# Performance work log

Measured on AMD Instinct MI355X. Metric: run time of the kernel, lower is better.

Reference implementation:

```python
import jax, jax.numpy as jnp
import numpy as np

B, W, H, I, L = 64, 4096, 128, 128, 2


def setup_inputs() -> dict:
    key = jax.random.key(0)
    ks = jax.random.split(key, 16)
    f = lambda k, s: jax.random.normal(k, s, dtype=jnp.float32) * 0.05
    return dict(
        input=f(ks[0], (B, 1, I)),
        h0=f(ks[1], (L, B, H)),
        c0=f(ks[2], (L, B, H)),
        encoder_output=f(ks[3], (B, W, H)),
        att_W=f(ks[4], (1, 2 * H)), att_b=f(ks[5], (1,)),
        inp_W=f(ks[6], (I, H + I)), inp_b=f(ks[7], (I,)),
        W_ih0=f(ks[8], (4 * H, I)), W_hh0=f(ks[9], (4 * H, H)),
        b_ih0=f(ks[10], (4 * H,)), b_hh0=f(ks[11], (4 * H,)),
        W_ih1=f(ks[12], (4 * H, H)), W_hh1=f(ks[13], (4 * H, H)),
        b_ih1=f(ks[14], (4 * H,)), b_hh1=f(ks[15], (4 * H,)),
    )


def _lstm_cell(x, h, c, W_ih, W_hh, b_ih, b_hh):
    # PyTorch gate order: i, f, g, o
    gates = x @ W_ih.T + h @ W_hh.T + b_ih + b_hh
    i, f, g, o = jnp.split(gates, 4, axis=-1)
    c_new = jax.nn.sigmoid(f) * c + jax.nn.sigmoid(i) * jnp.tanh(g)
    h_new = jax.nn.sigmoid(o) * jnp.tanh(c_new)
    return h_new, c_new


def reference(input, h0, c0, encoder_output, att_W, att_b, inp_W, inp_b,
              W_ih0, W_hh0, b_ih0, b_hh0, W_ih1, W_hh1, b_ih1, b_hh1):
    att_state = h0[-1] * c0[-1]                       # (B, H)
    # att_line over concat(enc_word, att_state): split the (1, 2H) weight.
    wa_enc, wa_st = att_W[0, :H], att_W[0, H:]
    scores = encoder_output @ wa_enc + (att_state @ wa_st + att_b[0])[:, None]  # (B, W)
    # Faithful to original: a leading zeros column is prepended, then
    # softmax is taken over [:, 0:-1] -> keeps the zero column, drops the
    # LAST word's score.
    zero_col = jnp.zeros((scores.shape[0], 1), scores.dtype)
    full = jnp.concatenate([zero_col, scores], axis=1)  # (B, W+1)
    weight = jax.nn.softmax(full[:, :-1], axis=1)        # (B, W)
    x = jnp.einsum('bw,bwh->bh', weight, encoder_output)  # (B, H)
    xin = jnp.concatenate([x, input[:, 0, :]], axis=1) @ inp_W.T + inp_b  # (B, I)
    # 2-layer LSTM, single time step (eval mode -> inter-layer dropout off)
    h1, c1 = _lstm_cell(xin, h0[0], c0[0], W_ih0, W_hh0, b_ih0, b_hh0)
    h2, c2 = _lstm_cell(h1, h0[1], c0[1], W_ih1, W_hh1, b_ih1, b_hh1)
    output = h2[:, None, :]                              # (B, 1, H)
    return output, jnp.stack([h1, h2]), jnp.stack([c1, c2])
```

## Files before the change

kernel.cpp:

```cpp
#include <hip/hip_runtime.h>

#define BB 64
#define WW 4096
#define HH 128
#define NCHUNK 32
#define CROWS 128
#define PSTRIDE 132

__device__ inline float sigmoidf(float x) { return 1.0f / (1.0f + expf(-x)); }

__global__ void fused_attention(const float* __restrict__ enc,
                                const float* __restrict__ h0,
                                const float* __restrict__ c0,
                                const float* __restrict__ attW,
                                const float* __restrict__ attb,
                                float* __restrict__ partials) {
    __shared__ float s_wa[128];
    __shared__ float s_red[128];
    __shared__ float s_sc[CROWS];
    __shared__ float s_p[CROWS];
    __shared__ float racc[16 * 128];
    __shared__ float s_bias, s_m, s_extra;

    const int t = threadIdx.x;
    const int b = blockIdx.x >> 5;
    const int chunk = blockIdx.x & 31;
    const int w0 = chunk * CROWS;

    const int seg = t & 15;
    const int rg  = t >> 4;

    float4 ra[8], rc[8];
#pragma unroll
    for (int pass = 0; pass < 8; pass++) {
        const int r = pass * 16 + rg;
        const float4* p = (const float4*)(enc + ((size_t)b * WW + w0 + r) * HH + seg * 8);
        ra[pass] = p[0];
        rc[pass] = p[1];
    }

    if (t < 128) {
        s_wa[t] = attW[t];
        float hv = h0[BB * HH + b * HH + t];
        float cv = c0[BB * HH + b * HH + t];
        s_red[t] = hv * cv * attW[HH + t];
    }
    __syncthreads();
    for (int s = 64; s > 0; s >>= 1) {
        if (t < s) s_red[t] += s_red[t + s];
        __syncthreads();
    }
    if (t == 0) s_bias = s_red[0] + attb[0];
    __syncthreads();
    const float bias = s_bias;

    float wseg[8];
#pragma unroll
    for (int j = 0; j < 8; j++) wseg[j] = s_wa[seg * 8 + j];

#pragma unroll
    for (int pass = 0; pass < 8; pass++) {
        const int r = pass * 16 + rg;
        float d = ra[pass].x * wseg[0] + ra[pass].y * wseg[1]
                + ra[pass].z * wseg[2] + ra[pass].w * wseg[3]
                + rc[pass].x * wseg[4] + rc[pass].y * wseg[5]
                + rc[pass].z * wseg[6] + rc[pass].w * wseg[7];
        d += __shfl_xor(d, 8, 16);
        d += __shfl_xor(d, 4, 16);
        d += __shfl_xor(d, 2, 16);
        d += __shfl_xor(d, 1, 16);
        if (seg == 0) s_sc[r] = d + bias;
    }

    if (chunk > 0 && t < 16) {
        const float4* p = (const float4*)(enc + ((size_t)b * WW + w0 - 1) * HH + t * 8);
        float4 a = p[0], c = p[1];
        float d = a.x * wseg[0] + a.y * wseg[1] + a.z * wseg[2] + a.w * wseg[3]
                + c.x * wseg[4] + c.y * wseg[5] + c.z * wseg[6] + c.w * wseg[7];
        d += __shfl_xor(d, 8, 16);
        d += __shfl_xor(d, 4, 16);
        d += __shfl_xor(d, 2, 16);
        d += __shfl_xor(d, 1, 16);
        if (t == 0) s_extra = d + bias;
    }
    __syncthreads();

    if (t < 128) {
        float v;
        if (t == 0) v = (chunk > 0) ? s_extra : -1e30f;
        else        v = s_sc[t - 1];
        s_p[t] = v;
    }
    __syncthreads();

    if (t < 64) s_red[t] = fmaxf(s_p[t], s_p[t + 64]);
    __syncthreads();
    for (int s = 32; s > 0; s >>= 1) {
        if (t < s) s_red[t] = fmaxf(s_red[t], s_red[t + s]);
        __syncthreads();
    }
    if (t == 0) s_m = s_red[0];
    __syncthreads();
    const float m = s_m;

    if (t < 128) s_p[t] = expf(s_p[t] - m);
    __syncthreads();
    if (t < 64) s_red[t] = s_p[t] + s_p[t + 64];
    __syncthreads();
    for (int s = 32; s > 0; s >>= 1) {
        if (t < s) s_red[t] += s_red[t + s];
        __syncthreads();
    }

    float acc8[8];
#pragma unroll
    for (int j = 0; j < 8; j++) acc8[j] = 0.f;
#pragma unroll
    for (int pass = 0; pass < 8; pass++) {
        const int r = pass * 16 + rg;
        const float pw = s_p[r];
        acc8[0] += pw * ra[pass].x; acc8[1] += pw * ra[pass].y;
        acc8[2] += pw * ra[pass].z; acc8[3] += pw * ra[pass].w;
        acc8[4] += pw * rc[pass].x; acc8[5] += pw * rc[pass].y;
        acc8[6] += pw * rc[pass].z; acc8[7] += pw * rc[pass].w;
    }
#pragma unroll
    for (int j = 0; j < 8; j++) racc[rg * 128 + seg * 8 + j] = acc8[j];
    __syncthreads();

    float* out = partials + (size_t)(b * NCHUNK + chunk) * PSTRIDE;
    if (t < 128) {
        float s = 0.f;
#pragma unroll
        for (int w2 = 0; w2 < 16; w2++) s += racc[w2 * 128 + t];
        out[t] = s;
    }
    if (t == 128) out[128] = m;
    if (t == 129) out[129] = s_red[0];
}

__global__ void tail_kernel(const float* __restrict__ partials,
                            const float* __restrict__ enc,
                            const float* __restrict__ input,
                            const float* __restrict__ inpW,
                            const float* __restrict__ inpb,
                            const float* __restrict__ Wih0,
                            const float* __restrict__ Whh0,
                            const float* __restrict__ bih0,
                            const float* __restrict__ bhh0,
                            const float* __restrict__ Wih1,
                            const float* __restrict__ Whh1,
                            const float* __restrict__ bih1,
                            const float* __restrict__ bhh1,
                            const float* __restrict__ h0,
                            const float* __restrict__ c0,
                            float* __restrict__ out) {
    __shared__ float lm[NCHUNK], llv[NCHUNK], ls[NCHUNK];
    __shared__ float sM, sL;
    __shared__ float xc[256];
    __shared__ float sxv[128];
    __shared__ float shv[128];
    __shared__ float sh1[128];
    __shared__ float shv2[128];
    __shared__ float gates[512];

    const int b = blockIdx.x;
    const int t = threadIdx.x;

    if (t < NCHUNK) {
        const float* pp = partials + (size_t)(b * NCHUNK + t) * PSTRIDE;
        lm[t] = pp[128];
        llv[t] = pp[129];
    }
    __syncthreads();
    if (t == 0) {
        float M = 0.0f;
        for (int c = 0; c < NCHUNK; c++) M = fmaxf(M, lm[c]);
        float L = expf(-M);
        for (int c = 0; c < NCHUNK; c++) {
            float s = expf(lm[c] - M);
            ls[c] = s;
            L += s * llv[c];
        }
        sM = M; sL = L;
    }
    __syncthreads();

    if (t < 128) {
        float xv = expf(-sM) * enc[(size_t)b * WW * HH + t];
        for (int c = 0; c < NCHUNK; c++)
            xv += ls[c] * partials[(size_t)(b * NCHUNK + c) * PSTRIDE + t];
        xc[t] = xv / sL;
        xc[128 + t] = input[b * HH + t];
    }
    __syncthreads();

    if (t < 128) {
        float a = inpb[t];
        const float4* wr = (const float4*)(inpW + (size_t)t * 256);
#pragma unroll
        for (int k = 0; k < 64; k++) {
            float4 w4 = wr[k];
            a += xc[4 * k] * w4.x + xc[4 * k + 1] * w4.y
               + xc[4 * k + 2] * w4.z + xc[4 * k + 3] * w4.w;
        }
        sxv[t] = a;
        shv[t] = h0[b * HH + t];
        shv2[t] = h0[BB * HH + b * HH + t];
    }
    __syncthreads();

    {
        float g = bih0[t] + bhh0[t];
        const float4* wi = (const float4*)(Wih0 + (size_t)t * 128);
        const float4* wh = (const float4*)(Whh0 + (size_t)t * 128);
#pragma unroll
        for (int k = 0; k < 32; k++) {
            float4 a = wi[k], c = wh[k];
            g += sxv[4 * k] * a.x + sxv[4 * k + 1] * a.y + sxv[4 * k + 2] * a.z + sxv[4 * k + 3] * a.w
               + shv[4 * k] * c.x + shv[4 * k + 1] * c.y + shv[4 * k + 2] * c.z + shv[4 * k + 3] * c.w;
        }
        gates[t] = g;
    }
    __syncthreads();
    if (t < 128) {
        float ig = sigmoidf(gates[t]);
        float fg = sigmoidf(gates[128 + t]);
        float gg = tanhf(gates[256 + t]);
        float og = sigmoidf(gates[384 + t]);
        float cn = fg * c0[b * HH + t] + ig * gg;
        float hn = og * tanhf(cn);
        out[8192 + b * HH + t] = hn;
        out[24576 + b * HH + t] = cn;
        sh1[t] = hn;
    }
    __syncthreads();

    {
        float g = bih1[t] + bhh1[t];
        const float4* wi = (const float4*)(Wih1 + (size_t)t * 128);
        const float4* wh = (const float4*)(Whh1 + (size_t)t * 128);
#pragma unroll
        for (int k = 0; k < 32; k++) {
            float4 a = wi[k], c = wh[k];
            g += sh1[4 * k] * a.x + sh1[4 * k + 1] * a.y + sh1[4 * k + 2] * a.z + sh1[4 * k + 3] * a.w
               + shv2[4 * k] * c.x + shv2[4 * k + 1] * c.y + shv2[4 * k + 2] * c.z + shv2[4 * k + 3] * c.w;
        }
        gates[t] = g;
    }
    __syncthreads();
    if (t < 128) {
        float ig = sigmoidf(gates[t]);
        float fg = sigmoidf(gates[128 + t]);
        float gg = tanhf(gates[256 + t]);
        float og = sigmoidf(gates[384 + t]);
        float cn = fg * c0[BB * HH + b * HH + t] + ig * gg;
        float hn = og * tanhf(cn);
        out[b * HH + t] = hn;
        out[16384 + b * HH + t] = hn;
        out[32768 + b * HH + t] = cn;
    }
}

extern "C" void kernel_launch(void* const* d_in, const int* in_sizes, int n_in,
                              void* d_out, int out_size, void* d_ws, size_t ws_size,
                              hipStream_t stream) {
    const float* input = (const float*)d_in[0];
    const float* h0    = (const float*)d_in[1];
    const float* c0    = (const float*)d_in[2];
    const float* enc   = (const float*)d_in[3];
    const float* attW  = (const float*)d_in[4];
    const float* attb  = (const float*)d_in[5];
    const float* inpW  = (const float*)d_in[6];
    const float* inpb  = (const float*)d_in[7];
    const float* Wih0  = (const float*)d_in[8];
    const float* Whh0  = (const float*)d_in[9];
    const float* bih0  = (const float*)d_in[10];
    const float* bhh0  = (const float*)d_in[11];
    const float* Wih1  = (const float*)d_in[12];
    const float* Whh1  = (const float*)d_in[13];
    const float* bih1  = (const float*)d_in[14];
    const float* bhh1  = (const float*)d_in[15];

    float* partials = (float*)d_ws;

    fused_attention<<<BB * NCHUNK, 256, 0, stream>>>(enc, h0, c0, attW, attb, partials);
    tail_kernel<<<BB, 512, 0, stream>>>(partials, enc, input, inpW, inpb,
                                        Wih0, Whh0, bih0, bhh0,
                                        Wih1, Whh1, bih1, bhh1,
                                        h0, c0, (float*)d_out);
}
```

Measured before the change: 273.4 us.

## Replace shared-memory tree reductions with wavefront shuffles and split tail work across threads

The attention kernel swaps its barrier-heavy shared-memory tree reductions (bias, max, sum) for 64-lane wavefront shuffle reductions, and shrinks the 16-row partial accumulation buffer by first reducing within each wave via shuffles. The halo-row load is issued early, next to the main loads. In the tail kernel, the per-chunk max and sum become a 32-lane shuffle reduction, and the chunk combine and input projection are split across all 512 threads with a small reduction, replacing 128-thread serial loops. The aim is to cut __syncthreads count and LDS traffic, and to make the tail less serial. The cost is extra shuffle instructions and more reduction steps.

```diff
diff --git a/kernel.cpp b/kernel.cpp
--- a/kernel.cpp
+++ b/kernel.cpp
@@ -16,11 +16,11 @@
                                 const float* __restrict__ attb,
                                 float* __restrict__ partials) {
     __shared__ float s_wa[128];
-    __shared__ float s_red[128];
+    __shared__ float s_red[8];
     __shared__ float s_sc[CROWS];
     __shared__ float s_p[CROWS];
-    __shared__ float racc[16 * 128];
-    __shared__ float s_bias, s_m, s_extra;
+    __shared__ float4 racc4[128];
+    __shared__ float s_extra;
 
     const int t = threadIdx.x;
     const int b = blockIdx.x >> 5;
@@ -29,6 +29,7 @@
 
     const int seg = t & 15;
     const int rg  = t >> 4;
+    const int wv  = t >> 6;
 
     float4 ra[8], rc[8];
 #pragma unroll
@@ -38,21 +39,28 @@
         ra[pass] = p[0];
         rc[pass] = p[1];
     }
+    float4 xa = {0.f,0.f,0.f,0.f}, xb = {0.f,0.f,0.f,0.f};
+    if (chunk > 0 && t < 16) {
+        const float4* p = (const float4*)(enc + ((size_t)b * WW + w0 - 1) * HH + t * 8);
+        xa = p[0];
+        xb = p[1];
+    }
 
     if (t < 128) {
         s_wa[t] = attW[t];
         float hv = h0[BB * HH + b * HH + t];
         float cv = c0[BB * HH + b * HH + t];
-        s_red[t] = hv * cv * attW[HH + t];
-    }
-    __syncthreads();
-    for (int s = 64; s > 0; s >>= 1) {
-        if (t < s) s_red[t] += s_red[t + s];
-        __syncthreads();
-    }
-    if (t == 0) s_bias = s_red[0] + attb[0];
-    __syncthreads();
-    const float bias = s_bias;
+        float r = hv * cv * attW[HH + t];
+        r += __shfl_xor(r, 32);
+        r += __shfl_xor(r, 16);
+        r += __shfl_xor(r, 8);
+        r += __shfl_xor(r, 4);
+        r += __shfl_xor(r, 2);
+        r += __shfl_xor(r, 1);
+        if ((t & 63) == 0) s_red[wv] = r;
+    }
+    __syncthreads();
+    const float bias = s_red[0] + s_red[1] + attb[0];
 
     float wseg[8];
 #pragma unroll
@@ -73,10 +81,8 @@
     }
 
     if (chunk > 0 && t < 16) {
-        const float4* p = (const float4*)(enc + ((size_t)b * WW + w0 - 1) * HH + t * 8);
-        float4 a = p[0], c = p[1];
-        float d = a.x * wseg[0] + a.y * wseg[1] + a.z * wseg[2] + a.w * wseg[3]
-                + c.x * wseg[4] + c.y * wseg[5] + c.z * wseg[6] + c.w * wseg[7];
+        float d = xa.x * wseg[0] + xa.y * wseg[1] + xa.z * wseg[2] + xa.w * wseg[3]
+                + xb.x * wseg[4] + xb.y * wseg[5] + xb.z * wseg[6] + xb.w * wseg[7];
         d += __shfl_xor(d, 8, 16);
         d += __shfl_xor(d, 4, 16);
         d += __shfl_xor(d, 2, 16);
@@ -85,32 +91,35 @@
     }
     __syncthreads();
 
-    if (t < 128) {
-        float v;
+    float v = -1e30f;
+    if (t < 128) {
         if (t == 0) v = (chunk > 0) ? s_extra : -1e30f;
         else        v = s_sc[t - 1];
-        s_p[t] = v;
-    }
-    __syncthreads();
-
-    if (t < 64) s_red[t] = fmaxf(s_p[t], s_p[t + 64]);
-    __syncthreads();
-    for (int s = 32; s > 0; s >>= 1) {
-        if (t < s) s_red[t] = fmaxf(s_red[t], s_red[t + s]);
-        __syncthreads();
-    }
-    if (t == 0) s_m = s_red[0];
-    __syncthreads();
-    const float m = s_m;
-
-    if (t < 128) s_p[t] = expf(s_p[t] - m);
-    __syncthreads();
-    if (t < 64) s_red[t] = s_p[t] + s_p[t + 64];
-    __syncthreads();
-    for (int s = 32; s > 0; s >>= 1) {
-        if (t < s) s_red[t] += s_red[t + s];
-        __syncthreads();
-    }
+        float mv = v;
+        mv = fmaxf(mv, __shfl_xor(mv, 32));
+        mv = fmaxf(mv, __shfl_xor(mv, 16));
+        mv = fmaxf(mv, __shfl_xor(mv, 8));
+        mv = fmaxf(mv, __shfl_xor(mv, 4));
+        mv = fmaxf(mv, __shfl_xor(mv, 2));
+        mv = fmaxf(mv, __shfl_xor(mv, 1));
+        if ((t & 63) == 0) s_red[2 + wv] = mv;
+    }
+    __syncthreads();
+    const float m = fmaxf(s_red[2], s_red[3]);
+
+    if (t < 128) {
+        float p = expf(v - m);
+        s_p[t] = p;
+        float sv = p;
+        sv += __shfl_xor(sv, 32);
+        sv += __shfl_xor(sv, 16);
+        sv += __shfl_xor(sv, 8);
+        sv += __shfl_xor(sv, 4);
+        sv += __shfl_xor(sv, 2);
+        sv += __shfl_xor(sv, 1);
+        if ((t & 63) == 0) s_red[4 + wv] = sv;
+    }
+    __syncthreads();
 
     float acc8[8];
 #pragma unroll
@@ -125,18 +134,27 @@
         acc8[6] += pw * rc[pass].z; acc8[7] += pw * rc[pass].w;
     }
 #pragma unroll
-    for (int j = 0; j < 8; j++) racc[rg * 128 + seg * 8 + j] = acc8[j];
+    for (int j = 0; j < 8; j++) {
+        acc8[j] += __shfl_xor(acc8[j], 16);
+        acc8[j] += __shfl_xor(acc8[j], 32);
+    }
+    if ((t & 63) < 16) {
+        float4 lo = {acc8[0], acc8[1], acc8[2], acc8[3]};
+        float4 hi = {acc8[4], acc8[5], acc8[6], acc8[7]};
+        racc4[wv * 32 + seg * 2 + 0] = lo;
+        racc4[wv * 32 + seg * 2 + 1] = hi;
+    }
     __syncthreads();
 
     float* out = partials + (size_t)(b * NCHUNK + chunk) * PSTRIDE;
     if (t < 128) {
-        float s = 0.f;
-#pragma unroll
-        for (int w2 = 0; w2 < 16; w2++) s += racc[w2 * 128 + t];
-        out[t] = s;
-    }
-    if (t == 128) out[128] = m;
-    if (t == 129) out[129] = s_red[0];
+        const float* rf = (const float*)racc4;
+        out[t] = rf[t] + rf[128 + t] + rf[256 + t] + rf[384 + t];
+    } else if (t == 128) {
+        out[128] = m;
+    } else if (t == 129) {
+        out[129] = s_red[4] + s_red[5];
+    }
 }
 
 __global__ void tail_kernel(const float* __restrict__ partials,
@@ -155,58 +173,86 @@
                             const float* __restrict__ h0,
                             const float* __restrict__ c0,
                             float* __restrict__ out) {
-    __shared__ float lm[NCHUNK], llv[NCHUNK], ls[NCHUNK];
+    __shared__ float lm[NCHUNK], ls[NCHUNK];
     __shared__ float sM, sL;
     __shared__ float xc[256];
     __shared__ float sxv[128];
     __shared__ float shv[128];
     __shared__ float sh1[128];
     __shared__ float shv2[128];
-    __shared__ float gates[512];
+    __shared__ float red4[512];
 
     const int b = blockIdx.x;
     const int t = threadIdx.x;
-
+    const int hc = t & 127;
+    const int q  = t >> 7;
+
+    float myllv = 0.f;
     if (t < NCHUNK) {
         const float* pp = partials + (size_t)(b * NCHUNK + t) * PSTRIDE;
         lm[t] = pp[128];
-        llv[t] = pp[129];
-    }
-    __syncthreads();
-    if (t == 0) {
-        float M = 0.0f;
-        for (int c = 0; c < NCHUNK; c++) M = fmaxf(M, lm[c]);
-        float L = expf(-M);
-        for (int c = 0; c < NCHUNK; c++) {
-            float s = expf(lm[c] - M);
-            ls[c] = s;
-            L += s * llv[c];
+        myllv = pp[129];
+    } else if (t >= 128 && t < 256) {
+        shv[hc] = h0[b * HH + hc];
+    } else if (t >= 256 && t < 384) {
+        shv2[hc] = h0[BB * HH + b * HH + hc];
+    } else if (t >= 384) {
+        xc[128 + hc] = input[b * HH + hc];
+    }
+    __syncthreads();
+
+    if (t < NCHUNK) {
+        float mv = lm[t];
+        mv = fmaxf(mv, __shfl_xor(mv, 16, 32));
+        mv = fmaxf(mv, __shfl_xor(mv, 8, 32));
+        mv = fmaxf(mv, __shfl_xor(mv, 4, 32));
+        mv = fmaxf(mv, __shfl_xor(mv, 2, 32));
+        mv = fmaxf(mv, __shfl_xor(mv, 1, 32));
+        mv = fmaxf(mv, 0.0f);
+        float s = expf(lm[t] - mv);
+        ls[t] = s;
+        float L = s * myllv;
+        L += __shfl_xor(L, 16, 32);
+        L += __shfl_xor(L, 8, 32);
+        L += __shfl_xor(L, 4, 32);
+        L += __shfl_xor(L, 2, 32);
+        L += __shfl_xor(L, 1, 32);
+        if (t == 0) { sM = mv; sL = L + expf(-mv); }
+    }
+    __syncthreads();
+
+    {
+        float xv = 0.f;
+#pragma unroll
+        for (int c = 0; c < 8; c++) {
+            const int cc = q * 8 + c;
+            xv += ls[cc] * partials[(size_t)(b * NCHUNK + cc) * PSTRIDE + hc];
         }
-        sM = M; sL = L;
-    }
-    __syncthreads();
-
-    if (t < 128) {
-        float xv = expf(-sM) * enc[(size_t)b * WW * HH + t];
-        for (int c = 0; c < NCHUNK; c++)
-            xv += ls[c] * partials[(size_t)(b * NCHUNK + c) * PSTRIDE + t];
-        xc[t] = xv / sL;
-        xc[128 + t] = input[b * HH + t];
-    }
-    __syncthreads();
-
-    if (t < 128) {
-        float a = inpb[t];
-        const float4* wr = (const float4*)(inpW + (size_t)t * 256);
-#pragma unroll
-        for (int k = 0; k < 64; k++) {
+        red4[t] = xv;
+    }
+    __syncthreads();
+    if (t < 128) {
+        float x = expf(-sM) * enc[(size_t)b * WW * HH + t]
+                + red4[t] + red4[128 + t] + red4[256 + t] + red4[384 + t];
+        xc[t] = x / sL;
+    }
+    __syncthreads();
+
+    {
+        float a = 0.f;
+        const float4* wr = (const float4*)(inpW + (size_t)hc * 256 + q * 64);
+#pragma unroll
+        for (int k = 0; k < 16; k++) {
             float4 w4 = wr[k];
-            a += xc[4 * k] * w4.x + xc[4 * k + 1] * w4.y
-               + xc[4 * k + 2] * w4.z + xc[4 * k + 3] * w4.w;
+            const int k0 = q * 64 + 4 * k;
+            a += xc[k0] * w4.x + xc[k0 + 1] * w4.y
+               + xc[k0 + 2] * w4.z + xc[k0 + 3] * w4.w;
         }
-        sxv[t] = a;
-        shv[t] = h0[b * HH + t];
-        shv2[t] = h0[BB * HH + b * HH + t];
+        red4[t] = a;
+    }
+    __syncthreads();
+    if (t < 128) {
+        sxv[t] = inpb[t] + red4[t] + red4[128 + t] + red4[256 + t] + red4[384 + t];
     }
     __syncthreads();
 
@@ -220,14 +266,14 @@
             g += sxv[4 * k] * a.x + sxv[4 * k + 1] * a.y + sxv[4 * k + 2] * a.z + sxv[4 * k + 3] * a.w
                + shv[4 * k] * c.x + shv[4 * k + 1] * c.y + shv[4 * k + 2] * c.z + shv[4 * k + 3] * c.w;
         }
-        gates[t] = g;
-    }
-    __syncthreads();
-    if (t < 128) {
-        float ig = sigmoidf(gates[t]);
-        float fg = sigmoidf(gates[128 + t]);
-        float gg = tanhf(gates[256 + t]);
-        float og = sigmoidf(gates[384 + t]);
+        red4[t] = g;
+    }
+    __syncthreads();
+    if (t < 128) {
+        float ig = sigmoidf(red4[t]);
+        float fg = sigmoidf(red4[128 + t]);
+        float gg = tanhf(red4[256 + t]);
+        float og = sigmoidf(red4[384 + t]);
         float cn = fg * c0[b * HH + t] + ig * gg;
         float hn = og * tanhf(cn);
         out[8192 + b * HH + t] = hn;
@@ -246,14 +292,14 @@
             g += sh1[4 * k] * a.x + sh1[4 * k + 1] * a.y + sh1[4 * k + 2] * a.z + sh1[4 * k + 3] * a.w
                + shv2[4 * k] * c.x + shv2[4 * k + 1] * c.y + shv2[4 * k + 2] * c.z + shv2[4 * k + 3] * c.w;
         }
-        gates[t] = g;
-    }
-    __syncthreads();
-    if (t < 128) {
-        float ig = sigmoidf(gates[t]);
-        float fg = sigmoidf(gates[128 + t]);
-        float gg = tanhf(gates[256 + t]);
-        float og = sigmoidf(gates[384 + t]);
+        red4[t] = g;
+    }
+    __syncthreads();
+    if (t < 128) {
+        float ig = sigmoidf(red4[t]);
+        float fg = sigmoidf(red4[128 + t]);
+        float gg = tanhf(red4[256 + t]);
+        float og = sigmoidf(red4[384 + t]);
         float cn = fg * c0[BB * HH + b * HH + t] + ig * gg;
         float hn = og * tanhf(cn);
         out[b * HH + t] = hn;
```

Result: no change. 271.0 us (-0.9%).
